# Performance work log

Hardware: AMD Instinct MI355X
Metric: run time of the kernel (lower is better)

## Reference

```python
import jax, jax.numpy as jnp
import numpy as np

B, S, HID = 4, 1024, 1024
H, HK, D = 16, 8, 64
EPS = 1e-6
THETA = 10000.0
ROPE_SCALE = 1.0


def _rms_norm(x, gamma=None):
    # RMSNorm over head_dim; Gemma-style (1+gamma) scale, v_norm has no scale.
    v = x * jax.lax.rsqrt(jnp.mean(x * x, axis=-1, keepdims=True) + EPS)
    return v if gamma is None else v * (1.0 + gamma)


def _rope_1d(x, pos, theta, scale):
    # x: [B,S,h,d], pos: [B,S] -> rotate-half RoPE along d
    d = x.shape[-1]
    inv_freq = 1.0 / (theta ** (jnp.arange(0, d, 2, dtype=jnp.float32) / d))  # [d/2]
    ang = (pos.astype(jnp.float32) / scale)[..., None] * inv_freq             # [B,S,d/2]
    cos = jnp.cos(ang)[:, :, None, :]
    sin = jnp.sin(ang)[:, :, None, :]
    x1, x2 = x[..., : d // 2], x[..., d // 2 :]
    return jnp.concatenate([x1 * cos - x2 * sin, x2 * cos + x1 * sin], axis=-1)


def _multidim_rope(x, positions_xy, theta, scale):
    # split head_dim in half: first half rotated by x-position, second by y-position
    d = x.shape[-1]
    xh, yh = x[..., : d // 2], x[..., d // 2 :]
    return jnp.concatenate(
        [_rope_1d(xh, positions_xy[..., 0], theta, scale),
         _rope_1d(yh, positions_xy[..., 1], theta, scale)], axis=-1)


def setup_inputs() -> dict:
    key = jax.random.key(0)
    ks = jax.random.split(key, 8)
    std = 0.02
    return {
        "hidden_states": jax.random.normal(ks[0], (B, S, HID), jnp.float32),
        "Wq": jax.random.normal(ks[1], (HID, H * D), jnp.float32) * std,
        "Wk": jax.random.normal(ks[2], (HID, HK * D), jnp.float32) * std,
        "Wv": jax.random.normal(ks[3], (HID, HK * D), jnp.float32) * std,
        "Wo": jax.random.normal(ks[4], (H * D, HID), jnp.float32) * std,
        "q_gamma": jax.random.normal(ks[5], (D,), jnp.float32) * 0.02,
        "k_gamma": jax.random.normal(ks[6], (D,), jnp.float32) * 0.02,
        "positions_xy": jax.random.randint(ks[7], (B, S, 2), 0, 32, dtype=jnp.int32),
        "attention_mask": jnp.ones((B, S, S), dtype=bool),
    }


def reference(hidden_states, Wq, Wk, Wv, Wo, q_gamma, k_gamma, positions_xy, attention_mask):
    b, s, _ = hidden_states.shape
    q = (hidden_states @ Wq).reshape(b, s, H, D)
    k = (hidden_states @ Wk).reshape(b, s, HK, D)
    v = (hidden_states @ Wv).reshape(b, s, HK, D)
    q = _rms_norm(q, q_gamma)
    k = _rms_norm(k, k_gamma)
    v = _rms_norm(v)  # no scale
    q = _multidim_rope(q, positions_xy, THETA, ROPE_SCALE).transpose(0, 2, 1, 3)  # [B,H,S,D]
    k = _multidim_rope(k, positions_xy, THETA, ROPE_SCALE).transpose(0, 2, 1, 3)  # [B,HK,S,D]
    v = v.transpose(0, 2, 1, 3)                                                   # [B,HK,S,D]
    groups = H // HK
    k = jnp.repeat(k, groups, axis=1)  # GQA expand -> [B,H,S,D]
    v = jnp.repeat(v, groups, axis=1)
    # scale=1.0 per the original SDPA call (no 1/sqrt(d))
    logits = jnp.einsum("bhqd,bhkd->bhqk", q, k)
    neg = jnp.asarray(jnp.finfo(logits.dtype).min, logits.dtype)
    logits = jnp.where(attention_mask[:, None, :, :], logits, neg)
    probs = jax.nn.softmax(logits.astype(jnp.float32), axis=-1).astype(q.dtype)
    out = jnp.einsum("bhqk,bhkd->bhqd", probs, v)
    out = out.transpose(0, 2, 1, 3).reshape(b, s, H * D)
    return out @ Wo
```

## Files before the change

kernel.cpp:

```cpp
#include <hip/hip_runtime.h>
#include <hip/hip_bf16.h>
#include <stdint.h>

typedef __attribute__((ext_vector_type(8))) short short8;
typedef __attribute__((ext_vector_type(4))) float f32x4;
typedef __attribute__((ext_vector_type(16))) float f32x16;

#define MFMA16(a, b, c) __builtin_amdgcn_mfma_f32_16x16x32_bf16(a, b, c, 0, 0, 0)
#define MFMA32(a, b, c) __builtin_amdgcn_mfma_f32_32x32x16_bf16(a, b, c, 0, 0, 0)

__device__ __forceinline__ unsigned short f2bf_u(float f) {
  union { float f; uint32_t u; } x; x.f = f;
  uint32_t r = (x.u + 0x7fffu + ((x.u >> 16) & 1u)) >> 16;
  return (unsigned short)r;
}
__device__ __forceinline__ short f2bf(float f) { return (short)f2bf_u(f); }

__device__ __forceinline__ uint32_t pack_bf2(float lo, float hi) {
  __hip_bfloat162 h = __float22bfloat162_rn(make_float2(lo, hi));
  union { __hip_bfloat162 h; uint32_t u; } c; c.h = h;
  return c.u;
}

__device__ __forceinline__ void gload_lds16(const void* g, void* lds) {
  __builtin_amdgcn_global_load_lds(
      (const __attribute__((address_space(1))) uint32_t*)(uintptr_t)g,
      (__attribute__((address_space(3))) uint32_t*)(uintptr_t)lds,
      16, 0, 0);
}

__global__ __launch_bounds__(256) void convert_bf16_kernel(
    const float* __restrict__ in, short* __restrict__ out, int n4) {
  int i = blockIdx.x * 256 + threadIdx.x;
  if (i >= n4) return;
  float4 v = reinterpret_cast<const float4*>(in)[i];
  short4 o;
  o.x = f2bf(v.x); o.y = f2bf(v.y); o.z = f2bf(v.z); o.w = f2bf(v.w);
  reinterpret_cast<short4*>(out)[i] = o;
}

__global__ __launch_bounds__(256) void transpose_all_kernel(
    const float* __restrict__ Wq, const float* __restrict__ Wk,
    const float* __restrict__ Wv, const float* __restrict__ Wo,
    short* __restrict__ WTQKV, short* __restrict__ WOT) {
  __shared__ float tile[32][33];
  int yb = blockIdx.y;
  const float* src; short* dst; int N; int yy;
  if (yb < 32)      { src = Wq; dst = WTQKV;                       N = 1024; yy = yb; }
  else if (yb < 48) { src = Wk; dst = WTQKV + (size_t)1024 * 1024; N = 512;  yy = yb - 32; }
  else if (yb < 64) { src = Wv; dst = WTQKV + (size_t)1536 * 1024; N = 512;  yy = yb - 48; }
  else              { src = Wo; dst = WOT;                         N = 1024; yy = yb - 64; }
  int k0 = blockIdx.x * 32, n0 = yy * 32;
  int tx = threadIdx.x, ty = threadIdx.y;
#pragma unroll
  for (int i = 0; i < 4; ++i)
    tile[ty + 8 * i][tx] = src[(size_t)(k0 + ty + 8 * i) * N + n0 + tx];
  __syncthreads();
#pragma unroll
  for (int i = 0; i < 4; ++i)
    dst[(size_t)(n0 + ty + 8 * i) * 1024 + k0 + tx] = f2bf(tile[tx][ty + 8 * i]);
}

__global__ __launch_bounds__(256) void gemm_qkv_fused(
    const short* __restrict__ A, const short* __restrict__ BT,
    const float* __restrict__ qg, const float* __restrict__ kg,
    const int* __restrict__ pos,
    short* __restrict__ Qp, short* __restrict__ Kp, short* __restrict__ Vt) {
  const int K = 1024;
  __shared__ short As[2 * 128 * 32];
  __shared__ short Bs[2 * 128 * 32];
  int wg = blockIdx.x + gridDim.x * blockIdx.y;
  int lid = (wg & 7) * 64 + (wg >> 3);
  int m0 = (lid & 31) * 128, n0 = (lid >> 5) * 128;
  int t = threadIdx.x;
  int w = t >> 6, lane = t & 63;
  int wr = w >> 1, wc = w & 1;
  int lr = lane & 15, lg = lane >> 4;

  f32x4 acc[4][4] = {};

  for (int k0 = 0; k0 < K; k0 += 64) {
    __syncthreads();
#pragma unroll
    for (int i = 0; i < 4; ++i) {
      int q = t + 256 * i;
      int kk = q >> 9, row = (q >> 2) & 127, c = q & 3;
      gload_lds16(A + (size_t)(m0 + row) * K + k0 + kk * 32 + c * 8, &As[q * 8]);
      gload_lds16(BT + (size_t)(n0 + row) * K + k0 + kk * 32 + c * 8, &Bs[q * 8]);
    }
    __syncthreads();
#pragma unroll
    for (int kk = 0; kk < 2; ++kk) {
      short8 af[4], bf[4];
#pragma unroll
      for (int mi = 0; mi < 4; ++mi)
        af[mi] = *(const short8*)&As[kk * 4096 + (wr * 64 + mi * 16 + lr) * 32 + lg * 8];
#pragma unroll
      for (int ni = 0; ni < 4; ++ni)
        bf[ni] = *(const short8*)&Bs[kk * 4096 + (wc * 64 + ni * 16 + lr) * 32 + lg * 8];
      __builtin_amdgcn_s_setprio(1);
#pragma unroll
      for (int mi = 0; mi < 4; ++mi)
#pragma unroll
        for (int ni = 0; ni < 4; ++ni)
          acc[mi][ni] = MFMA16(af[mi], bf[ni], acc[mi][ni]);
      __builtin_amdgcn_s_setprio(0);
    }
  }

  int g = (n0 >> 6) + wc;
  int row0 = m0 + wr * 64;
  const int2* posv = (const int2*)pos;

  if (g < 24) {
    const float* gsrc = (g < 16) ? qg : kg;
    short* dst = (g < 16) ? Qp : Kp;
    int nh = (g < 16) ? 16 : 8;
    int h = (g < 16) ? g : g - 16;
    float gscale = (g < 16) ? 1.4426950408889634f : 1.0f;
    float gam[4];
#pragma unroll
    for (int ni = 0; ni < 4; ++ni) gam[ni] = (1.0f + gsrc[ni * 16 + lr]) * gscale;
    float invf = exp2f((float)lr * -0.8304820237218405f);
#pragma unroll
    for (int mi = 0; mi < 4; ++mi) {
      f32x4 ss = acc[mi][0] * acc[mi][0];
#pragma unroll
      for (int ni = 1; ni < 4; ++ni) ss += acc[mi][ni] * acc[mi][ni];
#pragma unroll
      for (int m2 = 1; m2 < 16; m2 <<= 1)
#pragma unroll
        for (int r = 0; r < 4; ++r) ss[r] += __shfl_xor(ss[r], m2);
#pragma unroll
      for (int r = 0; r < 4; ++r) {
        int row = row0 + mi * 16 + lg * 4 + r;
        float inv = rsqrtf(ss[r] * 0.015625f + 1e-6f);
        float v0 = acc[mi][0][r] * inv * gam[0];
        float v1 = acc[mi][1][r] * inv * gam[1];
        float v2 = acc[mi][2][r] * inv * gam[2];
        float v3 = acc[mi][3][r] * inv * gam[3];
        int2 pp = posv[row];
        float sx, cx, sy, cy;
        __sincosf((float)pp.x * invf, &sx, &cx);
        __sincosf((float)pp.y * invf, &sy, &cy);
        float o0 = v0 * cx - v1 * sx, o1 = v1 * cx + v0 * sx;
        float o2 = v2 * cy - v3 * sy, o3 = v3 * cy + v2 * sy;
        int s = row & 1023, bb = row >> 10;
        short* base = dst + ((size_t)((bb * nh + h) * 1024 + s)) * 64;
        base[lr]      = f2bf(o0);
        base[lr + 16] = f2bf(o1);
        base[lr + 32] = f2bf(o2);
        base[lr + 48] = f2bf(o3);
      }
    }
  } else {
    int hk = g - 24;
#pragma unroll
    for (int mi = 0; mi < 4; ++mi) {
      f32x4 ss = acc[mi][0] * acc[mi][0];
#pragma unroll
      for (int ni = 1; ni < 4; ++ni) ss += acc[mi][ni] * acc[mi][ni];
#pragma unroll
      for (int m2 = 1; m2 < 16; m2 <<= 1)
#pragma unroll
        for (int r = 0; r < 4; ++r) ss[r] += __shfl_xor(ss[r], m2);
      f32x4 inv;
#pragma unroll
      for (int r = 0; r < 4; ++r) inv[r] = rsqrtf(ss[r] * 0.015625f + 1e-6f);
      int row = row0 + mi * 16 + lg * 4;
      int s0 = row & 1023, bb = row >> 10;
      int kv = s0 & 63, c = kv >> 3, hb = (kv >> 2) & 1;
      int sp = (s0 & ~63) | (((c & 6) | hb) << 3) | ((c & 1) << 2);
#pragma unroll
      for (int ni = 0; ni < 4; ++ni) {
        short4 sv;
        sv.x = f2bf(acc[mi][ni][0] * inv[0]);
        sv.y = f2bf(acc[mi][ni][1] * inv[1]);
        sv.z = f2bf(acc[mi][ni][2] * inv[2]);
        sv.w = f2bf(acc[mi][ni][3] * inv[3]);
        int d = ni * 16 + lr;
        *(short4*)&Vt[((size_t)((bb * 8 + hk) * 64 + d)) * 1024 + sp] = sv;
      }
    }
  }
}

__global__ __launch_bounds__(256) void gemm_bf16_bn64(
    const short* __restrict__ A, const short* __restrict__ BT,
    float* __restrict__ C, int M, int N, int K) {
  __shared__ short As[2 * 128 * 32];
  __shared__ short Bs[2 * 64 * 32];
  int wg = blockIdx.x + gridDim.x * blockIdx.y;
  int lid = (wg & 7) * 64 + (wg >> 3);
  int m0 = (lid & 31) * 128, n0 = (lid >> 5) * 64;
  int t = threadIdx.x;
  int w = t >> 6, lane = t & 63;
  int lr = lane & 15, lg = lane >> 4;

  f32x4 acc[2][4] = {};

  for (int k0 = 0; k0 < K; k0 += 64) {
    __syncthreads();
#pragma unroll
    for (int i = 0; i < 4; ++i) {
      int q = t + 256 * i;
      int kk = q >> 9, row = (q >> 2) & 127, c = q & 3;
      gload_lds16(A + (size_t)(m0 + row) * K + k0 + kk * 32 + c * 8, &As[q * 8]);
    }
#pragma unroll
    for (int i = 0; i < 2; ++i) {
      int q = t + 256 * i;
      int kk = q >> 8, row = (q >> 2) & 63, c = q & 3;
      gload_lds16(BT + (size_t)(n0 + row) * K + k0 + kk * 32 + c * 8, &Bs[q * 8]);
    }
    __syncthreads();
#pragma unroll
    for (int kk = 0; kk < 2; ++kk) {
      short8 af[2], bf[4];
#pragma unroll
      for (int mi = 0; mi < 2; ++mi)
        af[mi] = *(const short8*)&As[kk * 4096 + (w * 32 + mi * 16 + lr) * 32 + lg * 8];
#pragma unroll
      for (int ni = 0; ni < 4; ++ni)
        bf[ni] = *(const short8*)&Bs[kk * 2048 + (ni * 16 + lr) * 32 + lg * 8];
      __builtin_amdgcn_s_setprio(1);
#pragma unroll
      for (int mi = 0; mi < 2; ++mi)
#pragma unroll
        for (int ni = 0; ni < 4; ++ni)
          acc[mi][ni] = MFMA16(af[mi], bf[ni], acc[mi][ni]);
      __builtin_amdgcn_s_setprio(0);
    }
  }
#pragma unroll
  for (int mi = 0; mi < 2; ++mi)
#pragma unroll
    for (int ni = 0; ni < 4; ++ni) {
      int row = m0 + w * 32 + mi * 16 + lg * 4;
      int col = n0 + ni * 16 + lr;
#pragma unroll
      for (int r = 0; r < 4; ++r)
        C[(size_t)(row + r) * N + col] = acc[mi][ni][r];
    }
}

__global__ __launch_bounds__(128, 2) void attn_kernel(
    const short* __restrict__ Qp, const short* __restrict__ Kp,
    const short* __restrict__ Vt, short* __restrict__ attn) {
  __shared__ short Ks[2][4096];
  __shared__ short Vs[2][4096];
  int wg = blockIdx.x;
  int xcd = wg & 7, slot = wg >> 3;
  int group = xcd * 8 + (slot >> 4);
  int qblk = slot & 15;
  int b = group >> 4, h = group & 15;
  int hk = h >> 1;
  int t = threadIdx.x;
  int w = t >> 6, lane = t & 63;
  int l31 = lane & 31, hh = lane >> 5;
  int xr = l31 & 7;
  int q0 = qblk * 64 + w * 32;

  const short* Qb = Qp + ((size_t)(b * 16 + h) * 1024) * 64;
  const short* Kb = Kp + ((size_t)(b * 8 + hk) * 1024) * 64;
  const short* Vb = Vt + ((size_t)(b * 8 + hk) * 64) * 1024;

  short8 qf[4];
#pragma unroll
  for (int dk = 0; dk < 4; ++dk)
    qf[dk] = *(const short8*)&Qb[(q0 + l31) * 64 + dk * 16 + hh * 8];

  f32x16 acc[2] = {};
  f32x4 lsumv = {};

  auto STAGE = [&](short* ksb, short* vsb, int kt) {
    int kv0 = kt * 64;
#pragma unroll
    for (int i = 0; i < 4; ++i) {
      int q = t + 128 * i;
      int kv = q >> 3, cd = q & 7, cs = cd ^ (kv & 7);
      gload_lds16(Kb + (size_t)(kv0 + kv) * 64 + cs * 8, &ksb[q * 8]);
    }
#pragma unroll
    for (int i = 0; i < 4; ++i) {
      int q = t + 128 * i;
      int d = q >> 3, bi = q & 7, bs = bi ^ (d & 7);
      gload_lds16(Vb + (size_t)d * 1024 + kv0 + bs * 8, &vsb[q * 8]);
    }
  };

  auto COMPUTE = [&](const short* ksb, const short* vsb) {
#pragma unroll
    for (int kvb2 = 0; kvb2 < 2; ++kvb2) {
      short8 kf[4];
#pragma unroll
      for (int dk = 0; dk < 4; ++dk)
        kf[dk] = *(const short8*)&ksb[(kvb2 * 32 + l31) * 64 + ((dk * 2 + hh) ^ xr) * 8];
      f32x16 sv = {};
      __builtin_amdgcn_s_setprio(1);
#pragma unroll
      for (int dk = 0; dk < 4; ++dk) sv = MFMA32(kf[dk], qf[dk], sv);
      __builtin_amdgcn_s_setprio(0);
      short8 vf[4];
#pragma unroll
      for (int kvc = 0; kvc < 2; ++kvc)
#pragma unroll
        for (int db2 = 0; db2 < 2; ++db2)
          vf[kvc * 2 + db2] = *(const short8*)
              &vsb[(db2 * 32 + l31) * 64 + (((kvb2 * 4 + kvc * 2 + hh) ^ xr)) * 8];
      float p[16];
#pragma unroll
      for (int r = 0; r < 16; ++r) p[r] = exp2f(sv[r]);
#pragma unroll
      for (int r = 0; r < 16; r += 4) {
        lsumv[0] += p[r]; lsumv[1] += p[r + 1];
        lsumv[2] += p[r + 2]; lsumv[3] += p[r + 3];
      }
      uint32_t pk8[8];
#pragma unroll
      for (int j = 0; j < 8; ++j) pk8[j] = pack_bf2(p[2 * j], p[2 * j + 1]);
#pragma unroll
      for (int kvc = 0; kvc < 2; ++kvc) {
        union { uint32_t u[4]; short8 s; } pb;
#pragma unroll
        for (int j = 0; j < 4; ++j) pb.u[j] = pk8[kvc * 4 + j];
        __builtin_amdgcn_s_setprio(1);
#pragma unroll
        for (int db2 = 0; db2 < 2; ++db2)
          acc[db2] = MFMA32(vf[kvc * 2 + db2], pb.s, acc[db2]);
        __builtin_amdgcn_s_setprio(0);
      }
    }
  };

  STAGE(Ks[0], Vs[0], 0);
  int cur = 0;
  for (int kt = 0; kt < 15; ++kt) {
    STAGE(Ks[cur ^ 1], Vs[cur ^ 1], kt + 1);
    asm volatile("s_waitcnt vmcnt(8)" ::: "memory");
    __builtin_amdgcn_s_barrier();
    __builtin_amdgcn_sched_barrier(0);
    COMPUTE(Ks[cur], Vs[cur]);
    __builtin_amdgcn_sched_barrier(0);
    __builtin_amdgcn_s_barrier();
    cur ^= 1;
  }
  asm volatile("s_waitcnt vmcnt(0)" ::: "memory");
  __builtin_amdgcn_s_barrier();
  COMPUTE(Ks[cur], Vs[cur]);

  float lsum = (lsumv[0] + lsumv[1]) + (lsumv[2] + lsumv[3]);
  lsum += __shfl_xor(lsum, 32);
  float inv = 1.0f / lsum;
  short* orow = attn + ((size_t)(b * 1024 + q0 + l31)) * 1024 + h * 64;
#pragma unroll
  for (int db2 = 0; db2 < 2; ++db2)
#pragma unroll
    for (int g2 = 0; g2 < 4; ++g2) {
      int d0 = db2 * 32 + g2 * 8 + 4 * hh;
      uint32_t w0 = pack_bf2(acc[db2][g2 * 4 + 0] * inv, acc[db2][g2 * 4 + 1] * inv);
      uint32_t w1 = pack_bf2(acc[db2][g2 * 4 + 2] * inv, acc[db2][g2 * 4 + 3] * inv);
      *(uint2*)&orow[d0] = make_uint2(w0, w1);
    }
}

extern "C" void kernel_launch(void* const* d_in, const int* in_sizes, int n_in,
                              void* d_out, int out_size, void* d_ws, size_t ws_size,
                              hipStream_t stream) {
  const float* X  = (const float*)d_in[0];
  const float* Wq = (const float*)d_in[1];
  const float* Wk = (const float*)d_in[2];
  const float* Wv = (const float*)d_in[3];
  const float* Wo = (const float*)d_in[4];
  const float* qg = (const float*)d_in[5];
  const float* kg = (const float*)d_in[6];
  const int* pos  = (const int*)d_in[7];
  float* out = (float*)d_out;

  char* ws = (char*)d_ws;
  short* XB    = (short*)(ws);
  short* WTQKV = (short*)(ws + ((size_t)8 << 20));
  short* WOT   = (short*)(ws + ((size_t)12 << 20));
  short* QP    = (short*)(ws + ((size_t)14 << 20));
  short* KP    = (short*)(ws + ((size_t)22 << 20));
  short* VT    = (short*)(ws + ((size_t)26 << 20));
  short* ATT   = (short*)(ws + ((size_t)30 << 20));

  convert_bf16_kernel<<<4096, 256, 0, stream>>>(X, XB, 1048576);
  transpose_all_kernel<<<dim3(32, 96), dim3(32, 8), 0, stream>>>(Wq, Wk, Wv, Wo, WTQKV, WOT);

  gemm_qkv_fused<<<dim3(32, 16), 256, 0, stream>>>(XB, WTQKV, qg, kg, pos, QP, KP, VT);
  attn_kernel<<<1024, 128, 0, stream>>>(QP, KP, VT, ATT);
  gemm_bf16_bn64<<<dim3(32, 16), 256, 0, stream>>>(ATT, WOT, out, 4096, 1024, 1024);
}
```

Baseline: 99.30 us.

## Split attention KV range across two wave pairs and reduce partials in LDS

The attention kernel doubles its workgroup to 256 threads. Each query wave pair now processes one half of the 1024-key sequence with its own double-buffered K/V tiles, cutting the sequential loop from 16 to 8 iterations. Partial output accumulators and row sums from the second KV half are combined through shared memory before normalisation and the store. This raises parallelism per query block, at the cost of 64KB of LDS per block, which may limit occupancy, plus an extra reduction step with synchronisation. The softmax appears to use no running max (unnormalised exp with a plain sum), so partials can be added directly.

Result: no change. 99.24 us (-0.1%).

```diff
diff --git a/kernel.cpp b/kernel.cpp
--- a/kernel.cpp
+++ b/kernel.cpp
@@ -244,11 +244,11 @@
     }
 }
 
-__global__ __launch_bounds__(128, 2) void attn_kernel(
+__global__ __launch_bounds__(256, 2) void attn_kernel(
     const short* __restrict__ Qp, const short* __restrict__ Kp,
     const short* __restrict__ Vt, short* __restrict__ attn) {
-  __shared__ short Ks[2][4096];
-  __shared__ short Vs[2][4096];
+  __shared__ char smem[65536];
+  __shared__ float lsl[2][32][2];
   int wg = blockIdx.x;
   int xcd = wg & 7, slot = wg >> 3;
   int group = xcd * 8 + (slot >> 4);
@@ -257,9 +257,10 @@
   int hk = h >> 1;
   int t = threadIdx.x;
   int w = t >> 6, lane = t & 63;
+  int qw = w >> 1, kw = w & 1;
   int l31 = lane & 31, hh = lane >> 5;
   int xr = l31 & 7;
-  int q0 = qblk * 64 + w * 32;
+  int q0 = qblk * 64 + qw * 32;
 
   const short* Qb = Qp + ((size_t)(b * 16 + h) * 1024) * 64;
   const short* Kb = Kp + ((size_t)(b * 8 + hk) * 1024) * 64;
@@ -273,23 +274,30 @@
   f32x16 acc[2] = {};
   f32x4 lsumv = {};
 
-  auto STAGE = [&](short* ksb, short* vsb, int kt) {
-    int kv0 = kt * 64;
+  auto KsB = [&](int buf) { return (short*)(smem + (size_t)(kw * 2 + buf) * 8192); };
+  auto VsB = [&](int buf) { return (short*)(smem + 32768 + (size_t)(kw * 2 + buf) * 8192); };
+
+  auto STAGE = [&](int buf, int kt) {
+    int kv0 = kw * 512 + kt * 64;
+    short* ksb = KsB(buf);
+    short* vsb = VsB(buf);
 #pragma unroll
     for (int i = 0; i < 4; ++i) {
-      int q = t + 128 * i;
-      int kv = q >> 3, cd = q & 7, cs = cd ^ (kv & 7);
-      gload_lds16(Kb + (size_t)(kv0 + kv) * 64 + cs * 8, &ksb[q * 8]);
+      int c = i * 128 + qw * 64 + lane;
+      int kv = c >> 3, cd = c & 7, cs = cd ^ (kv & 7);
+      gload_lds16(Kb + (size_t)(kv0 + kv) * 64 + cs * 8, &ksb[c * 8]);
     }
 #pragma unroll
     for (int i = 0; i < 4; ++i) {
-      int q = t + 128 * i;
-      int d = q >> 3, bi = q & 7, bs = bi ^ (d & 7);
-      gload_lds16(Vb + (size_t)d * 1024 + kv0 + bs * 8, &vsb[q * 8]);
+      int c = i * 128 + qw * 64 + lane;
+      int d = c >> 3, bi = c & 7, bs = bi ^ (d & 7);
+      gload_lds16(Vb + (size_t)d * 1024 + kv0 + bs * 8, &vsb[c * 8]);
     }
   };
 
-  auto COMPUTE = [&](const short* ksb, const short* vsb) {
+  auto COMPUTE = [&](int buf) {
+    const short* ksb = KsB(buf);
+    const short* vsb = VsB(buf);
 #pragma unroll
     for (int kvb2 = 0; kvb2 < 2; ++kvb2) {
       short8 kf[4];
@@ -333,35 +341,66 @@
     }
   };
 
-  STAGE(Ks[0], Vs[0], 0);
+  STAGE(0, 0);
   int cur = 0;
-  for (int kt = 0; kt < 15; ++kt) {
-    STAGE(Ks[cur ^ 1], Vs[cur ^ 1], kt + 1);
+  for (int kt = 0; kt < 7; ++kt) {
+    STAGE(cur ^ 1, kt + 1);
     asm volatile("s_waitcnt vmcnt(8)" ::: "memory");
     __builtin_amdgcn_s_barrier();
     __builtin_amdgcn_sched_barrier(0);
-    COMPUTE(Ks[cur], Vs[cur]);
+    COMPUTE(cur);
     __builtin_amdgcn_sched_barrier(0);
     __builtin_amdgcn_s_barrier();
     cur ^= 1;
   }
   asm volatile("s_waitcnt vmcnt(0)" ::: "memory");
   __builtin_amdgcn_s_barrier();
-  COMPUTE(Ks[cur], Vs[cur]);
+  COMPUTE(cur);
 
   float lsum = (lsumv[0] + lsumv[1]) + (lsumv[2] + lsumv[3]);
-  lsum += __shfl_xor(lsum, 32);
-  float inv = 1.0f / lsum;
-  short* orow = attn + ((size_t)(b * 1024 + q0 + l31)) * 1024 + h * 64;
-#pragma unroll
-  for (int db2 = 0; db2 < 2; ++db2)
-#pragma unroll
-    for (int g2 = 0; g2 < 4; ++g2) {
-      int d0 = db2 * 32 + g2 * 8 + 4 * hh;
-      uint32_t w0 = pack_bf2(acc[db2][g2 * 4 + 0] * inv, acc[db2][g2 * 4 + 1] * inv);
-      uint32_t w1 = pack_bf2(acc[db2][g2 * 4 + 2] * inv, acc[db2][g2 * 4 + 3] * inv);
-      *(uint2*)&orow[d0] = make_uint2(w0, w1);
-    }
+  __syncthreads();
+  float* accl = (float*)smem;
+  float* ab = accl + (((qw * 32 + l31) * 2 + hh) * 36);
+  if (kw == 1) {
+#pragma unroll
+    for (int db2 = 0; db2 < 2; ++db2)
+#pragma unroll
+      for (int j4 = 0; j4 < 4; ++j4) {
+        f32x4 sv4;
+        sv4[0] = acc[db2][j4 * 4];
+        sv4[1] = acc[db2][j4 * 4 + 1];
+        sv4[2] = acc[db2][j4 * 4 + 2];
+        sv4[3] = acc[db2][j4 * 4 + 3];
+        *(f32x4*)&ab[db2 * 16 + j4 * 4] = sv4;
+      }
+    lsl[qw][l31][hh] = lsum;
+  }
+  __syncthreads();
+  if (kw == 0) {
+#pragma unroll
+    for (int db2 = 0; db2 < 2; ++db2)
+#pragma unroll
+      for (int j4 = 0; j4 < 4; ++j4) {
+        f32x4 o = *(const f32x4*)&ab[db2 * 16 + j4 * 4];
+        acc[db2][j4 * 4]     += o[0];
+        acc[db2][j4 * 4 + 1] += o[1];
+        acc[db2][j4 * 4 + 2] += o[2];
+        acc[db2][j4 * 4 + 3] += o[3];
+      }
+    lsum += lsl[qw][l31][hh];
+    lsum += __shfl_xor(lsum, 32);
+    float inv = 1.0f / lsum;
+    short* orow = attn + ((size_t)(b * 1024 + q0 + l31)) * 1024 + h * 64;
+#pragma unroll
+    for (int db2 = 0; db2 < 2; ++db2)
+#pragma unroll
+      for (int g2 = 0; g2 < 4; ++g2) {
+        int d0 = db2 * 32 + g2 * 8 + 4 * hh;
+        uint32_t w0 = pack_bf2(acc[db2][g2 * 4 + 0] * inv, acc[db2][g2 * 4 + 1] * inv);
+        uint32_t w1 = pack_bf2(acc[db2][g2 * 4 + 2] * inv, acc[db2][g2 * 4 + 3] * inv);
+        *(uint2*)&orow[d0] = make_uint2(w0, w1);
+      }
+  }
 }
 
 extern "C" void kernel_launch(void* const* d_in, const int* in_sizes, int n_in,
@@ -390,6 +429,6 @@
   transpose_all_kernel<<<dim3(32, 96), dim3(32, 8), 0, stream>>>(Wq, Wk, Wv, Wo, WTQKV, WOT);
 
   gemm_qkv_fused<<<dim3(32, 16), 256, 0, stream>>>(XB, WTQKV, qg, kg, pos, QP, KP, VT);
-  attn_kernel<<<1024, 128, 0, stream>>>(QP, KP, VT, ATT);
+  attn_kernel<<<1024, 256, 0, stream>>>(QP, KP, VT, ATT);
   gemm_bf16_bn64<<<dim3(32, 16), 256, 0, stream>>>(ATT, WOT, out, 4096, 1024, 1024);
 }
```
